# Optimization experiments

Measured on AMD Instinct MI355X. Metric: run time of the kernel, lower is better.

The kernel has to match this reference:

```python
import jax, jax.numpy as jnp
import numpy as np

N = 50000
E = 800000
D = 128          # in_dim = hid_dim = out_dim
R = 8            # num_rels
B = 8            # num_bases
N_LAYERS = 2


def _rgcn_conv(x, basis, comp, root, bias, src, dst, etype):
    """One PyG-style RGCNConv with basis decomposition, mean aggregation per
    relation, root (self-loop) weight and bias.
    x: [N, Din]; basis: [B, Din, Dout]; comp: [R, B]; root: [Din, Dout]; bias: [Dout].
    """
    n = x.shape[0]
    # Relation weights from basis decomposition: W[r] = sum_b comp[r,b] * basis[b]
    W = jnp.einsum('rb,bio->rio', comp, basis)           # [R, Din, Dout]
    # Transform every node under every relation, then gather per-edge message.
    H = jnp.einsum('ni,rio->nro', x, W)                  # [N, R, Dout]
    msg = H[src, etype]                                  # [E, Dout]
    # Per-(dst, relation) in-degree for mean aggregation (PyG aggr='mean').
    deg = jnp.zeros((n, R), x.dtype).at[dst, etype].add(1.0)
    inv = 1.0 / jnp.maximum(deg[dst, etype], 1.0)        # [E]
    agg = jnp.zeros((n, W.shape[2]), x.dtype).at[dst].add(msg * inv[:, None])
    return agg + x @ root + bias


def setup_inputs() -> dict:
    key = jax.random.key(0)
    ks = jax.random.split(key, 3 + 4 * N_LAYERS)
    x = jax.random.normal(ks[0], (N, D), dtype=jnp.float32)
    edge_index = jax.random.randint(ks[1], (2, E), 0, N, dtype=jnp.int64)
    edge_type = jax.random.randint(ks[2], (E,), 0, R, dtype=jnp.int64)
    inp = {'x': x, 'edge_index': edge_index, 'edge_type': edge_type}
    scale = 1.0 / np.sqrt(D)
    for l in range(N_LAYERS):
        k0, k1, k2 = ks[3 + 4 * l], ks[4 + 4 * l], ks[5 + 4 * l]
        inp[f'basis{l}'] = jax.random.normal(k0, (B, D, D), dtype=jnp.float32) * scale
        inp[f'comp{l}'] = jax.random.normal(k1, (R, B), dtype=jnp.float32) * (1.0 / np.sqrt(B))
        inp[f'root{l}'] = jax.random.normal(k2, (D, D), dtype=jnp.float32) * scale
        inp[f'bias{l}'] = jnp.zeros((D,), dtype=jnp.float32)
    return inp


def reference(x, edge_index, edge_type,
              basis0, comp0, root0, bias0,
              basis1, comp1, root1, bias1):
    src, dst = edge_index[0], edge_index[1]
    etype = edge_type
    h = _rgcn_conv(x, basis0, comp0, root0, bias0, src, dst, etype)
    h = jax.nn.relu(h)                 # activation between layers (dropout=0.0)
    h = _rgcn_conv(h, basis1, comp1, root1, bias1, src, dst, etype)
    return h
```

## Files before the change

### kernel.cpp

```cpp
#include <hip/hip_runtime.h>

#define NN 50000
#define EE 800000
#define DD 128
#define RR 8
#define KSTACK 1152
#define NR2 (NN * RR)
#define RPB 16
#define ROWB 2304
#define DUMP16 2304

typedef __attribute__((ext_vector_type(8))) short bf16x8;
typedef __attribute__((ext_vector_type(4))) float f32x4;

__device__ inline float bf2f(ushort u) {
    union { uint i; float f; } v; v.i = ((uint)u) << 16; return v.f;
}
__device__ inline ushort f2bf(float f) {
    uint b = __float_as_uint(f);
    uint r = (b + 0x7fffu + ((b >> 16) & 1u)) >> 16;
    return (ushort)r;
}

__global__ void __launch_bounds__(256) k_build_w3(
        const float* __restrict__ b0, const float* __restrict__ c0,
        const float* __restrict__ r0, const float* __restrict__ b1,
        const float* __restrict__ c1, const float* __restrict__ r1,
        ushort* __restrict__ w0, ushort* __restrict__ w1) {
    __shared__ float tile[32][132];
    const float* basis = blockIdx.y ? b1 : b0;
    const float* comp  = blockIdx.y ? c1 : c0;
    const float* root  = blockIdx.y ? r1 : r0;
    ushort* wT         = blockIdx.y ? w1 : w0;
    int tid = threadIdx.x;
    int k0 = blockIdx.x * 32;
    #pragma unroll
    for (int it = 0; it < 16; ++it) {
        int idx = it * 256 + tid;
        int kk = idx >> 7, o = idx & 127;
        int k = k0 + kk;
        float val;
        if (k < RR * DD) {
            int r = k >> 7, i = k & 127;
            float s = 0.f;
            #pragma unroll
            for (int b = 0; b < 8; ++b) s += comp[r * 8 + b] * basis[(b * 128 + i) * 128 + o];
            val = s;
        } else {
            val = root[(k - RR * DD) * 128 + o];
        }
        tile[kk][o] = val;
    }
    __syncthreads();
    int o = tid >> 1, half = tid & 1;
    ushort* wp = wT + (size_t)o * KSTACK + k0 + half * 16;
    #pragma unroll
    for (int j = 0; j < 8; ++j) {
        float lo = tile[half * 16 + 2 * j][o];
        float hi = tile[half * 16 + 2 * j + 1][o];
        uint pk;
        asm("v_cvt_pk_bf16_f32 %0, %1, %2" : "=v"(pk) : "v"(lo), "v"(hi));
        *(uint*)(wp + 2 * j) = pk;
    }
}

__global__ void k_cvt_bf16(const float* __restrict__ x, ushort* __restrict__ xb, int n4) {
    int i = blockIdx.x * 256 + threadIdx.x;
    if (i < n4) {
        float4 v = ((const float4*)x)[i];
        uint2 p;
        p.x = (uint)f2bf(v.x) | ((uint)f2bf(v.y) << 16);
        p.y = (uint)f2bf(v.z) | ((uint)f2bf(v.w) << 16);
        ((uint2*)xb)[i] = p;
    }
}

__global__ void k_hist(const int* __restrict__ ei, const int* __restrict__ et,
                       int* __restrict__ deg_dr) {
    int e = blockIdx.x * 256 + threadIdx.x;
    if (e < EE) atomicAdd(&deg_dr[ei[EE + e] * RR + et[e]], 1);
}

__device__ inline int rowdeg(const int* __restrict__ deg_dr, int n) {
    int4 a = ((const int4*)deg_dr)[2 * n];
    int4 b = ((const int4*)deg_dr)[2 * n + 1];
    return a.x + a.y + a.z + a.w + b.x + b.y + b.z + b.w;
}

__global__ void k_scan1(const int* __restrict__ deg_dr, int* __restrict__ bsum, int n) {
    __shared__ int s[256];
    int t = threadIdx.x;
    int i = blockIdx.x * 256 + t;
    s[t] = (i < n) ? rowdeg(deg_dr, i) : 0;
    __syncthreads();
    for (int o = 128; o > 0; o >>= 1) {
        if (t < o) s[t] += s[t + o];
        __syncthreads();
    }
    if (t == 0) bsum[blockIdx.x] = s[0];
}

__global__ void k_scan2(int* __restrict__ bsum, int nb) {
    __shared__ int s[256];
    int t = threadIdx.x;
    int v = (t < nb) ? bsum[t] : 0;
    s[t] = v;
    __syncthreads();
    for (int o = 1; o < 256; o <<= 1) {
        int u = (t >= o) ? s[t - o] : 0;
        __syncthreads();
        s[t] += u;
        __syncthreads();
    }
    if (t < nb) bsum[t] = s[t] - v;
}

__global__ void k_scan3(const int* __restrict__ deg_dr, const int* __restrict__ boff,
                        int* __restrict__ ptr, int n) {
    __shared__ int s[256];
    int t = threadIdx.x;
    int i = blockIdx.x * 256 + t;
    int v = (i < n) ? rowdeg(deg_dr, i) : 0;
    s[t] = v;
    __syncthreads();
    for (int o = 1; o < 256; o <<= 1) {
        int u = (t >= o) ? s[t - o] : 0;
        __syncthreads();
        s[t] += u;
        __syncthreads();
    }
    if (i < n) ptr[i + 1] = boff[blockIdx.x] + s[t];
    if (i == 0) ptr[0] = 0;
}

__global__ void k_scatter(const int* __restrict__ ei, const int* __restrict__ et,
                          const int* __restrict__ row_ptr, const int* __restrict__ deg_dr,
                          int* __restrict__ cursor, int2* __restrict__ ekw) {
    int e = blockIdx.x * 256 + threadIdx.x;
    if (e < EE) {
        int s = ei[e], d = ei[EE + e], t = et[e];
        int4 a = ((const int4*)deg_dr)[2 * d];
        int4 b = ((const int4*)deg_dr)[2 * d + 1];
        int pre = 0;
        pre += (t > 0) ? a.x : 0; pre += (t > 1) ? a.y : 0;
        pre += (t > 2) ? a.z : 0; pre += (t > 3) ? a.w : 0;
        pre += (t > 4) ? b.x : 0; pre += (t > 5) ? b.y : 0;
        pre += (t > 6) ? b.z : 0;
        int deg = (t == 0) ? a.x : (t == 1) ? a.y : (t == 2) ? a.z : (t == 3) ? a.w
                : (t == 4) ? b.x : (t == 5) ? b.y : (t == 6) ? b.z : b.w;
        int p = row_ptr[d] + pre + atomicAdd(&cursor[d * RR + t], 1);
        int lrow = d & (RPB - 1);
        int base16 = lrow * (ROWB >> 4) + t * 16;
        int2 pk;
        pk.x = (base16 << 19) | ((lrow & 7) << 16) | s;
        pk.y = __float_as_int(1.f / (float)deg);
        ekw[p] = pk;
    }
}

__global__ void __launch_bounds__(512, 8) k_fused5(
        const ushort* __restrict__ in, const int* __restrict__ rp,
        const int2* __restrict__ ekw, const ushort* __restrict__ BT,
        const float* __restrict__ bias, ushort* __restrict__ hout,
        float* __restrict__ fout) {
    __shared__ uint4 at4[(RPB * ROWB + 256) / 16];
    char* atb = (char*)at4;
    int tid = threadIdx.x, wid = tid >> 6, lane = tid & 63;
    int blockrow = blockIdx.x * RPB;
    uint lane4 = (uint)lane << 2;

    {
        uint4 z = {0u, 0u, 0u, 0u};
        for (int i = tid; i < (RPB * ROWB + 256) / 16; i += 512) at4[i] = z;
    }
    __syncthreads();

    const ushort* inl = in + (lane << 1);

    #pragma unroll
    for (int rr = 0; rr < 2; ++rr) {
        int lr = (wid << 1) + rr;
        int n = blockrow + lr;
        if (n < NN) {
            uint su = *(const uint*)(inl + (size_t)n * DD);
            uint off = (uint)(lr * ROWB + 2048) + (lane4 ^ ((uint)(lr & 7) << 4));
            *(uint*)(atb + off) = su;
        }
    }

    int n0 = blockrow + (wid << 1);
    int i0 = n0 < NN ? n0 : NN;
    int i1 = n0 + 2 < NN ? n0 + 2 : NN;
    int p    = __builtin_amdgcn_readfirstlane(rp[i0]);
    int pend = __builtin_amdgcn_readfirstlane(rp[i1]);
    int nb = pend - p;

    const int U = 8;
    int2 kA[U], kB[U];
    uint gA[U], gB[U];
    float a0 = 0.f, a1 = 0.f;
    uint prev = 0xFFFFFFFFu;

    auto loadc = [&](int2* kb, uint* gb, int base) {
        #pragma unroll
        for (int j = 0; j < U; ++j) {
            int pe = base + j;
            bool dummy = pe >= pend;
            pe = dummy ? (pend - 1) : pe;
            int2 e = ekw[pe];
            if (dummy) { e.x = (int)((uint)DUMP16 << 19); e.y = 0; }
            kb[j] = e;
        }
        #pragma unroll
        for (int j = 0; j < U; ++j)
            gb[j] = *(const uint*)(inl + ((size_t)(kb[j].x & 0xFFFF)) * DD);
    };
    auto proc = [&](int2* kb, uint* gb) {
        #pragma unroll
        for (int j = 0; j < U; ++j) {
            uint ex = (uint)kb[j].x;
            float w = __int_as_float(kb[j].y);
            uint off = ((ex >> 19) << 4) + (lane4 ^ ((ex >> 12) & 0x70u));
            bool same = (off == prev);
            a0 = same ? a0 : 0.f;
            a1 = same ? a1 : 0.f;
            uint g = gb[j];
            a0 += w * bf2f((ushort)(g & 0xFFFFu));
            a1 += w * bf2f((ushort)(g >> 16));
            uint pk;
            asm("v_cvt_pk_bf16_f32 %0, %1, %2" : "=v"(pk) : "v"(a0), "v"(a1));
            *(uint*)(atb + off) = pk;
            prev = off;
        }
    };

    if (nb > 0) {
        int nch = (nb + U - 1) / U;
        loadc(kA, gA, p);
        int i = 1;
        for (; i + 1 < nch; i += 2) {
            loadc(kB, gB, p + i * U);
            proc(kA, gA);
            loadc(kA, gA, p + (i + 1) * U);
            proc(kB, gB);
        }
        if (i < nch) {
            loadc(kB, gB, p + i * U);
            proc(kA, gA);
            proc(kB, gB);
        } else {
            proc(kA, gA);
        }
    }
    __syncthreads();

    int rlo = lane & 15, q = lane >> 4;
    int colbase = wid << 4;
    uint x7 = (uint)(rlo & 7) << 4;
    const char* arow = atb + rlo * ROWB;
    const ushort* bp = BT + (size_t)(colbase + rlo) * KSTACK + (q << 3);
    f32x4 c0 = {0.f, 0.f, 0.f, 0.f};
    #pragma unroll 4
    for (int kk = 0; kk < KSTACK / 32; ++kk) {
        uint loff = (uint)(kk * 64 + q * 16) ^ x7;
        bf16x8 b  = *(const bf16x8*)(bp + kk * 32);
        bf16x8 af = *(const bf16x8*)(arow + loff);
        c0 = __builtin_amdgcn_mfma_f32_16x16x32_bf16(af, b, c0, 0, 0, 0);
    }
    int col = colbase + rlo;
    float bv = bias[col];
    int rowoff = q << 2;
    #pragma unroll
    for (int rg = 0; rg < 4; ++rg) {
        int row = blockrow + rowoff + rg;
        if (row < NN) {
            float v = c0[rg] + bv;
            if (hout) {
                v = fmaxf(v, 0.f);
                hout[(size_t)row * DD + col] = f2bf(v);
            } else {
                fout[(size_t)row * DD + col] = v;
            }
        }
    }
}

extern "C" void kernel_launch(void* const* d_in, const int* in_sizes, int n_in,
                              void* d_out, int out_size, void* d_ws, size_t ws_size,
                              hipStream_t stream) {
    const float* x      = (const float*)d_in[0];
    const int*   ei     = (const int*)d_in[1];
    const int*   et     = (const int*)d_in[2];
    const float* basis0 = (const float*)d_in[3];
    const float* comp0  = (const float*)d_in[4];
    const float* root0  = (const float*)d_in[5];
    const float* bias0  = (const float*)d_in[6];
    const float* basis1 = (const float*)d_in[7];
    const float* comp1  = (const float*)d_in[8];
    const float* root1  = (const float*)d_in[9];
    const float* bias1  = (const float*)d_in[10];
    float* out = (float*)d_out;

    char* ws = (char*)d_ws;
    size_t off = 0;
    auto alloc = [&](size_t bytes) -> void* {
        void* p = ws + off;
        off += (bytes + 255) & ~(size_t)255;
        return p;
    };
    int*    deg_dr  = (int*)alloc((size_t)NR2 * 4);
    int*    cursor  = (int*)alloc((size_t)NR2 * 4);
    size_t zero_bytes = off;
    int*    row_ptr = (int*)alloc((size_t)(NN + 1) * 4);
    int*    bsum    = (int*)alloc(256 * 4);
    int2*   ekw     = (int2*)alloc((size_t)EE * 8);
    ushort* wT0     = (ushort*)alloc((size_t)DD * KSTACK * 2);
    ushort* wT1     = (ushort*)alloc((size_t)DD * KSTACK * 2);
    ushort* xb      = (ushort*)alloc((size_t)NN * DD * 2);
    ushort* h       = (ushort*)alloc((size_t)NN * DD * 2);
    if (off > ws_size) return;

    hipMemsetAsync(d_ws, 0, zero_bytes, stream);

    dim3 wgrid(KSTACK / 32, 2);
    k_build_w3<<<wgrid, 256, 0, stream>>>(basis0, comp0, root0, basis1, comp1, root1, wT0, wT1);
    k_cvt_bf16<<<6250, 256, 0, stream>>>(x, xb, NN * DD / 4);
    k_hist<<<3125, 256, 0, stream>>>(ei, et, deg_dr);
    k_scan1<<<196, 256, 0, stream>>>(deg_dr, bsum, NN);
    k_scan2<<<1, 256, 0, stream>>>(bsum, 196);
    k_scan3<<<196, 256, 0, stream>>>(deg_dr, bsum, row_ptr, NN);
    k_scatter<<<3125, 256, 0, stream>>>(ei, et, row_ptr, deg_dr, cursor, ekw);

    int fblocks = NN / RPB;
    k_fused5<<<fblocks, 512, 0, stream>>>(xb, row_ptr, ekw, wT0, bias0, h, nullptr);
    k_fused5<<<fblocks, 512, 0, stream>>>(h, row_ptr, ekw, wT1, bias1, nullptr, out);
}
```

Baseline: 346.5 us.

## Halve fused block to 4 waves, each gathering 4 rows and computing 32 output columns

The fused gather+MFMA kernel now runs with 256 threads instead of 512. Each wave handles four destination rows in the edge-gather phase and two 16-column MFMA tiles in the GEMM phase, so each LDS A-fragment load feeds two MFMAs. Bounds checks on rows are removed because NN is a multiple of RPB, and s_setprio raises wave priority around the MFMA loop. The trade-off is fewer waves per block for latency hiding in the gather, and more registers per thread from the doubled accumulators.

```diff
diff --git a/kernel.cpp b/kernel.cpp
--- a/kernel.cpp
+++ b/kernel.cpp
@@ -8,6 +8,7 @@
 #define NR2 (NN * RR)
 #define RPB 16
 #define ROWB 2304
+#define DUMPB 36864u
 #define DUMP16 2304
 
 typedef __attribute__((ext_vector_type(8))) short bf16x8;
@@ -158,7 +159,7 @@
     }
 }
 
-__global__ void __launch_bounds__(512, 8) k_fused5(
+__global__ void __launch_bounds__(256, 4) k_fused7(
         const ushort* __restrict__ in, const int* __restrict__ rp,
         const int2* __restrict__ ekw, const ushort* __restrict__ BT,
         const float* __restrict__ bias, ushort* __restrict__ hout,
@@ -171,28 +172,24 @@
 
     {
         uint4 z = {0u, 0u, 0u, 0u};
-        for (int i = tid; i < (RPB * ROWB + 256) / 16; i += 512) at4[i] = z;
+        for (int i = tid; i < (RPB * ROWB + 256) / 16; i += 256) at4[i] = z;
     }
     __syncthreads();
 
     const ushort* inl = in + (lane << 1);
 
     #pragma unroll
-    for (int rr = 0; rr < 2; ++rr) {
-        int lr = (wid << 1) + rr;
+    for (int rr = 0; rr < 4; ++rr) {
+        int lr = (wid << 2) + rr;
         int n = blockrow + lr;
-        if (n < NN) {
-            uint su = *(const uint*)(inl + (size_t)n * DD);
-            uint off = (uint)(lr * ROWB + 2048) + (lane4 ^ ((uint)(lr & 7) << 4));
-            *(uint*)(atb + off) = su;
-        }
-    }
-
-    int n0 = blockrow + (wid << 1);
-    int i0 = n0 < NN ? n0 : NN;
-    int i1 = n0 + 2 < NN ? n0 + 2 : NN;
-    int p    = __builtin_amdgcn_readfirstlane(rp[i0]);
-    int pend = __builtin_amdgcn_readfirstlane(rp[i1]);
+        uint su = *(const uint*)(inl + (size_t)n * DD);
+        uint off = (uint)(lr * ROWB + 2048) + (lane4 ^ ((uint)(lr & 7) << 4));
+        *(uint*)(atb + off) = su;
+    }
+
+    int n0 = blockrow + (wid << 2);
+    int p    = __builtin_amdgcn_readfirstlane(rp[n0]);
+    int pend = __builtin_amdgcn_readfirstlane(rp[n0 + 4]);
     int nb = pend - p;
 
     const int U = 8;
@@ -255,32 +252,37 @@
     __syncthreads();
 
     int rlo = lane & 15, q = lane >> 4;
-    int colbase = wid << 4;
+    int colbase = wid << 5;
     uint x7 = (uint)(rlo & 7) << 4;
     const char* arow = atb + rlo * ROWB;
-    const ushort* bp = BT + (size_t)(colbase + rlo) * KSTACK + (q << 3);
-    f32x4 c0 = {0.f, 0.f, 0.f, 0.f};
+    const ushort* bp0 = BT + (size_t)(colbase + rlo) * KSTACK + (q << 3);
+    const ushort* bp1 = bp0 + (size_t)16 * KSTACK;
+    f32x4 c0 = {0.f, 0.f, 0.f, 0.f}, c1 = {0.f, 0.f, 0.f, 0.f};
+    __builtin_amdgcn_s_setprio(1);
     #pragma unroll 4
     for (int kk = 0; kk < KSTACK / 32; ++kk) {
         uint loff = (uint)(kk * 64 + q * 16) ^ x7;
-        bf16x8 b  = *(const bf16x8*)(bp + kk * 32);
         bf16x8 af = *(const bf16x8*)(arow + loff);
-        c0 = __builtin_amdgcn_mfma_f32_16x16x32_bf16(af, b, c0, 0, 0, 0);
-    }
-    int col = colbase + rlo;
-    float bv = bias[col];
+        bf16x8 b0 = *(const bf16x8*)(bp0 + kk * 32);
+        bf16x8 b1 = *(const bf16x8*)(bp1 + kk * 32);
+        c0 = __builtin_amdgcn_mfma_f32_16x16x32_bf16(af, b0, c0, 0, 0, 0);
+        c1 = __builtin_amdgcn_mfma_f32_16x16x32_bf16(af, b1, c1, 0, 0, 0);
+    }
+    __builtin_amdgcn_s_setprio(0);
+    int col0 = colbase + rlo, col1 = col0 + 16;
+    float bv0 = bias[col0], bv1 = bias[col1];
     int rowoff = q << 2;
     #pragma unroll
     for (int rg = 0; rg < 4; ++rg) {
         int row = blockrow + rowoff + rg;
-        if (row < NN) {
-            float v = c0[rg] + bv;
-            if (hout) {
-                v = fmaxf(v, 0.f);
-                hout[(size_t)row * DD + col] = f2bf(v);
-            } else {
-                fout[(size_t)row * DD + col] = v;
-            }
+        float v0 = c0[rg] + bv0, v1 = c1[rg] + bv1;
+        if (hout) {
+            v0 = fmaxf(v0, 0.f); v1 = fmaxf(v1, 0.f);
+            hout[(size_t)row * DD + col0] = f2bf(v0);
+            hout[(size_t)row * DD + col1] = f2bf(v1);
+        } else {
+            fout[(size_t)row * DD + col0] = v0;
+            fout[(size_t)row * DD + col1] = v1;
         }
     }
 }
@@ -332,6 +334,6 @@
     k_scatter<<<3125, 256, 0, stream>>>(ei, et, row_ptr, deg_dr, cursor, ekw);
 
     int fblocks = NN / RPB;
-    k_fused5<<<fblocks, 512, 0, stream>>>(xb, row_ptr, ekw, wT0, bias0, h, nullptr);
-    k_fused5<<<fblocks, 512, 0, stream>>>(h, row_ptr, ekw, wT1, bias1, nullptr, out);
-}
+    k_fused7<<<fblocks, 256, 0, stream>>>(xb, row_ptr, ekw, wT0, bias0, h, nullptr);
+    k_fused7<<<fblocks, 256, 0, stream>>>(h, row_ptr, ekw, wT1, bias1, nullptr, out);
+}
```

After: 357.2 us. 1.03x slower.
